# Performance work log

Measured on AMD Instinct MI355X. Metric: run time of the kernel, lower is better.

The kernel has to match this reference:

```python
import jax, jax.numpy as jnp
import numpy as np

N = 100000      # nodes
E = 1600000     # edges
F_IN = 512      # num_features
H = 128         # hidden
C = 40          # num_classes
K = 10          # Chebyshev order


def setup_inputs() -> dict:
    key = jax.random.key(0)
    ks = jax.random.split(key, 6)
    x = jax.random.normal(ks[0], (N, F_IN), dtype=jnp.float32)
    edge_index = jax.random.randint(ks[1], (2, E), 0, N, dtype=jnp.int32)
    W1 = jax.random.normal(ks[2], (F_IN, H), dtype=jnp.float32) / np.sqrt(F_IN).astype(np.float32)
    b1 = jnp.zeros((H,), dtype=jnp.float32)
    W2 = jax.random.normal(ks[3], (H, C), dtype=jnp.float32) / np.sqrt(H).astype(np.float32)
    b2 = jnp.zeros((C,), dtype=jnp.float32)
    # Chebyshev coefficients temp[K+1]
    temp = 1.0 + 0.1 * jax.random.normal(ks[4], (K + 1,), dtype=jnp.float32)
    return {"x": x, "edge_index": edge_index, "W1": W1, "b1": b1, "W2": W2, "b2": b2, "temp": temp}


def reference(x, edge_index, W1, b1, W2, b2, temp):
    # MLP encoder (eval mode: dropout is identity)
    h = jax.nn.relu(x @ W1 + b1)          # [N, H]
    h = h @ W2 + b2                        # [N, C]

    # gcn_norm: add self-loops, symmetric normalization
    self_loop = jnp.arange(N, dtype=edge_index.dtype)
    row = jnp.concatenate([edge_index[0], self_loop])   # [E+N]
    col = jnp.concatenate([edge_index[1], self_loop])
    deg = jax.ops.segment_sum(jnp.ones_like(row, dtype=jnp.float32), row, num_segments=N)
    dis = jnp.where(deg > 0, jax.lax.rsqrt(jnp.maximum(deg, 1.0)), 0.0)
    norm = dis[row] * dis[col]             # [E+N]

    def prop(v):  # A_hat @ v : gather-scale-scatter over edges
        return jax.ops.segment_sum(norm[:, None] * v[col], row, num_segments=N)

    # Chebyshev recurrence: Tx_k = 2*A_hat*Tx_{k-1} - Tx_{k-2}
    Tx0 = h
    Tx1 = prop(h)
    out0 = temp[0] * Tx0 + temp[1] * Tx1

    def body(carry, coe):
        t0, t1, acc = carry
        t2 = 2.0 * prop(t1) - t0
        return (t1, t2, acc + coe * t2), None

    (_, _, out), _ = jax.lax.scan(body, (Tx0, Tx1, out0), temp[2:])
    return jax.nn.log_softmax(out, axis=1)
```

## Files before the change

### kernel.cpp

```cpp
#include <hip/hip_runtime.h>
#include <hip/hip_bf16.h>
#include <cstdint>
#include <cstddef>

#define NN   100000
#define EE   1600000
#define FIN  512
#define HID  128
#define CC   40
#define KORD 10
#define SHB  80
#define SHSTRIDE ((size_t)NN * SHB)

typedef __attribute__((ext_vector_type(4))) float f4;
typedef __attribute__((ext_vector_type(8))) short short8_t;
typedef __attribute__((ext_vector_type(4))) unsigned int u4;

__device__ __forceinline__ unsigned short cvt_bf16(float f) {
  union { float f; unsigned u; } a; a.f = f;
  unsigned r = a.u + 0x7fffu + ((a.u >> 16) & 1u);
  return (unsigned short)(r >> 16);
}
__device__ __forceinline__ unsigned pk_bf(float a, float b) {
  union { float f; unsigned u; } x, y; x.f = a; y.f = b;
  unsigned ra = x.u + 0x7fffu + ((x.u >> 16) & 1u);
  unsigned rb = y.u + 0x7fffu + ((y.u >> 16) & 1u);
  return (ra >> 16) | (rb & 0xffff0000u);
}
__device__ __forceinline__ f4 cvf2(unsigned lo, unsigned hi) {
  union { unsigned u; float f; } a, b, c, d;
  a.u = lo << 16; b.u = lo & 0xffff0000u;
  c.u = hi << 16; d.u = hi & 0xffff0000u;
  f4 r; r.x = a.f; r.y = b.f; r.z = c.f; r.w = d.f; return r;
}

__global__ __launch_bounds__(256) void k_dw(const int* __restrict__ rowI, int* __restrict__ deg,
                                            const float* __restrict__ W1, unsigned short* __restrict__ W1T,
                                            int ndeg) {
  int b = blockIdx.x;
  if (b < ndeg) {
    int i = b * 256 + threadIdx.x;
    if (i < EE) atomicAdd(&deg[rowI[i]], 1);
  } else {
    int idx = (b - ndeg) * 256 + threadIdx.x;
    int k = idx >> 7, n = idx & 127;
    W1T[(k >> 5) * 4096 + n * 32 + (k & 31)] = cvt_bf16(W1[idx]);
  }
}

__global__ __launch_bounds__(256) void k_finalize(int* __restrict__ deg, float* __restrict__ dis,
                                                  float* __restrict__ sqd, float* __restrict__ invd) {
  int i = blockIdx.x * 256 + threadIdx.x;
  if (i < NN) {
    int d = deg[i] + 1;
    deg[i] = d;
    float fd = (float)d;
    dis[i]  = rsqrtf(fd);
    sqd[i]  = sqrtf(fd);
    invd[i] = 1.0f / fd;
  }
}

__global__ __launch_bounds__(256) void k_scan1(const int* __restrict__ cnt, int* __restrict__ excl,
                                               int* __restrict__ bsums) {
  __shared__ int s[256];
  int tid = threadIdx.x;
  int base = blockIdx.x * 1024 + tid * 4;
  int v0 = (base + 0 < NN) ? cnt[base + 0] : 0;
  int v1 = (base + 1 < NN) ? cnt[base + 1] : 0;
  int v2 = (base + 2 < NN) ? cnt[base + 2] : 0;
  int v3 = (base + 3 < NN) ? cnt[base + 3] : 0;
  int tsum = v0 + v1 + v2 + v3;
  s[tid] = tsum;
  __syncthreads();
  for (int off = 1; off < 256; off <<= 1) {
    int t = (tid >= off) ? s[tid - off] : 0;
    __syncthreads();
    if (tid >= off) s[tid] += t;
    __syncthreads();
  }
  int run = s[tid] - tsum;
  if (tid == 255) bsums[blockIdx.x] = s[255];
  if (base + 0 < NN) excl[base + 0] = run; run += v0;
  if (base + 1 < NN) excl[base + 1] = run; run += v1;
  if (base + 2 < NN) excl[base + 2] = run; run += v2;
  if (base + 3 < NN) excl[base + 3] = run;
}

__global__ __launch_bounds__(128) void k_scan2(int* __restrict__ bsums, int nb) {
  __shared__ int s[128];
  int tid = threadIdx.x;
  int v = (tid < nb) ? bsums[tid] : 0;
  s[tid] = v;
  __syncthreads();
  for (int off = 1; off < 128; off <<= 1) {
    int t = (tid >= off) ? s[tid - off] : 0;
    __syncthreads();
    if (tid >= off) s[tid] += t;
    __syncthreads();
  }
  if (tid < nb) bsums[tid] = s[tid] - v;
}

__global__ __launch_bounds__(256) void k_scan3(const int* __restrict__ cnt, int* __restrict__ rs,
                                               int* __restrict__ cur, const int* __restrict__ bsums) {
  int i = blockIdx.x * 256 + threadIdx.x;
  if (i < NN) {
    int v = rs[i] + bsums[i >> 10];
    rs[i] = v;
    cur[i] = v;
    if (i == NN - 1) rs[NN] = v + cnt[i];
  }
}

#define SLICE_ROWS (NN / 8)
#define SC_CHUNK   2048
__global__ __launch_bounds__(256) void k_scatter(const int* __restrict__ rowI, const int* __restrict__ colI,
                                                 int* __restrict__ cur, int* __restrict__ colS) {
  int slice = blockIdx.x & 7;
  int chunk = blockIdx.x >> 3;
  int lo = slice * SLICE_ROWS, hi = lo + SLICE_ROWS;
#pragma unroll
  for (int t = 0; t < SC_CHUNK / 256; ++t) {
    int i = chunk * SC_CHUNK + t * 256 + threadIdx.x;
    if (i < EE + NN) {
      int r = (i < EE) ? rowI[i] : (i - EE);
      if (r >= lo && r < hi) {
        int c = (i < EE) ? colI[i] : r;
        int pos = atomicAdd(&cur[r], 1);
        colS[pos] = c * SHB;
      }
    }
  }
}

#define LDK 40
__global__ __launch_bounds__(256) void k_gemm1(const float* __restrict__ x, const unsigned short* __restrict__ W1T,
                                               const float* __restrict__ b1, float* __restrict__ h1) {
  __shared__ __align__(16) short As_s[128][LDK];
  __shared__ __align__(16) short Bs_s[128][LDK];
  int tid  = threadIdx.x;
  int wave = tid >> 6, lane = tid & 63;
  int blockRow = blockIdx.x * 128;
  int wr = (wave & 1) * 64, wc = (wave >> 1) * 64;
  int l15 = lane & 15, lk = (lane >> 4) * 8;
  int ar = tid >> 1, ak = (tid & 1) * 16;

  f4 acc[4][4] = {};

  for (int k0 = 0; k0 < FIN; k0 += 32) {
    int gr = blockRow + ar;
    f4 xv0 = {0.f,0.f,0.f,0.f}, xv1 = xv0, xv2 = xv0, xv3 = xv0;
    if (gr < NN) {
      const float* xr = x + (size_t)gr * FIN + k0 + ak;
      xv0 = *(const f4*)&xr[0];
      xv1 = *(const f4*)&xr[4];
      xv2 = *(const f4*)&xr[8];
      xv3 = *(const f4*)&xr[12];
    }
    short8_t p0, p1;
#pragma unroll
    for (int q = 0; q < 4; ++q) {
      p0[q]     = (short)cvt_bf16(xv0[q]);
      p0[q + 4] = (short)cvt_bf16(xv1[q]);
      p1[q]     = (short)cvt_bf16(xv2[q]);
      p1[q + 4] = (short)cvt_bf16(xv3[q]);
    }
    *(short8_t*)&As_s[ar][ak]     = p0;
    *(short8_t*)&As_s[ar][ak + 8] = p1;

    const unsigned short* Wt = W1T + (k0 >> 5) * 4096;
    short8_t q0 = *(const short8_t*)&Wt[tid * 16];
    short8_t q1 = *(const short8_t*)&Wt[tid * 16 + 8];
    int bn = tid >> 1, bkk = (tid & 1) * 16;
    *(short8_t*)&Bs_s[bn][bkk]     = q0;
    *(short8_t*)&Bs_s[bn][bkk + 8] = q1;

    __syncthreads();

    short8_t afr[4], bfr[4];
#pragma unroll
    for (int m = 0; m < 4; ++m) afr[m] = *(const short8_t*)&As_s[wr + m * 16 + l15][lk];
#pragma unroll
    for (int n = 0; n < 4; ++n) bfr[n] = *(const short8_t*)&Bs_s[wc + n * 16 + l15][lk];
#pragma unroll
    for (int m = 0; m < 4; ++m)
#pragma unroll
      for (int n = 0; n < 4; ++n)
        acc[m][n] = __builtin_amdgcn_mfma_f32_16x16x32_bf16(afr[m], bfr[n], acc[m][n], 0, 0, 0);

    __syncthreads();
  }

  float bias[4];
#pragma unroll
  for (int n = 0; n < 4; ++n) bias[n] = b1[wc + n * 16 + l15];
#pragma unroll
  for (int m = 0; m < 4; ++m) {
    int baseRow = blockRow + wr + m * 16 + (lane >> 4) * 4;
#pragma unroll
    for (int n = 0; n < 4; ++n) {
      int col = wc + n * 16 + l15;
#pragma unroll
      for (int r = 0; r < 4; ++r) {
        int grow = baseRow + r;
        if (grow < NN) h1[(size_t)grow * HID + col] = fmaxf(acc[m][n][r] + bias[n], 0.f);
      }
    }
  }
}

__global__ __launch_bounds__(256) void k_gemm2(const float* __restrict__ h1, const float* __restrict__ W2,
                                               const float* __restrict__ b2, const float* __restrict__ temp,
                                               const float* __restrict__ dis,
                                               unsigned short* __restrict__ sh0) {
  __shared__ float sW[HID * CC];
  __shared__ float sb[CC];
  int tid = threadIdx.x;
  for (int i = tid; i < HID * CC; i += 256) sW[i] = W2[i];
  if (tid < CC) sb[tid] = b2[tid];
  __syncthreads();
  int gid = blockIdx.x * 256 + tid;
  if (gid >= NN * 20) return;
  int row = gid / 20;
  int c2  = (gid - row * 20) * 2;
  const float* hr = h1 + (size_t)row * HID;
  float a0 = sb[c2], a1 = sb[c2 + 1];
#pragma unroll 8
  for (int k = 0; k < HID; ++k) {
    float hv = hr[k];
    a0 = fmaf(hv, sW[k * CC + c2], a0);
    a1 = fmaf(hv, sW[k * CC + c2 + 1], a1);
  }
  float dv = dis[row];
  *(unsigned*)((char*)sh0 + (size_t)row * SHB + c2 * 2) = pk_bf(a0 * dv, a1 * dv);
}

template <int MODE>
__global__ __launch_bounds__(256) void k_prop(const unsigned short* __restrict__ shIn,
                                              const unsigned short* __restrict__ shPrev,
                                              unsigned short* __restrict__ shOut,
                                              const int* __restrict__ colS,
                                              const int* __restrict__ rs,
                                              const float* __restrict__ invd) {
  int lane = threadIdx.x & 63;
  int wave = threadIdx.x >> 6;
  int grp  = lane / 5;
  int fi   = lane - grp * 5;
  int node = blockIdx.x * 48 + wave * 12 + grp;
  bool active = (grp < 12) && (node < NN);
  int s = 0, e = 0;
  if (active) { s = rs[node]; e = rs[node + 1]; }
  const char* base = (const char*)shIn + fi * 16;
  f4 lo0 = {0.f,0.f,0.f,0.f}, hi0 = lo0, lo1 = lo0, hi1 = lo0;
  f4 lo2 = lo0, hi2 = lo0, lo3 = lo0, hi3 = lo0;
  int j = s;
  for (; j + 4 <= e; j += 4) {
    int c0 = colS[j], c1 = colS[j + 1], c2 = colS[j + 2], c3 = colS[j + 3];
    u4 p0 = *(const u4*)(base + c0);
    u4 p1 = *(const u4*)(base + c1);
    u4 p2 = *(const u4*)(base + c2);
    u4 p3 = *(const u4*)(base + c3);
    lo0 += cvf2(p0.x, p0.y); hi0 += cvf2(p0.z, p0.w);
    lo1 += cvf2(p1.x, p1.y); hi1 += cvf2(p1.z, p1.w);
    lo2 += cvf2(p2.x, p2.y); hi2 += cvf2(p2.z, p2.w);
    lo3 += cvf2(p3.x, p3.y); hi3 += cvf2(p3.z, p3.w);
  }
  if (j + 2 <= e) {
    int c0 = colS[j], c1 = colS[j + 1];
    u4 p0 = *(const u4*)(base + c0);
    u4 p1 = *(const u4*)(base + c1);
    lo0 += cvf2(p0.x, p0.y); hi0 += cvf2(p0.z, p0.w);
    lo1 += cvf2(p1.x, p1.y); hi1 += cvf2(p1.z, p1.w);
    j += 2;
  }
  if (j < e) {
    u4 p0 = *(const u4*)(base + colS[j]);
    lo2 += cvf2(p0.x, p0.y); hi2 += cvf2(p0.z, p0.w);
  }

  if (active) {
    f4 slo = (lo0 + lo1) + (lo2 + lo3);
    f4 shi = (hi0 + hi1) + (hi2 + hi3);
    float iv = invd[node];
    size_t ro = (size_t)node * SHB + fi * 16;
    f4 wlo, whi;
    if (MODE == 0) {
      wlo = iv * slo; whi = iv * shi;
    } else {
      u4 pp = *(const u4*)((const char*)shPrev + ro);
      f4 plo = cvf2(pp.x, pp.y), phi = cvf2(pp.z, pp.w);
      wlo = (2.f * iv) * slo - plo;
      whi = (2.f * iv) * shi - phi;
    }
    u4 pk;
    pk.x = pk_bf(wlo.x, wlo.y); pk.y = pk_bf(wlo.z, wlo.w);
    pk.z = pk_bf(whi.x, whi.y); pk.w = pk_bf(whi.z, whi.w);
    *(u4*)((char*)shOut + ro) = pk;
  }
}

__global__ __launch_bounds__(256) void k_comb(const unsigned short* __restrict__ shBase,
                                              float* __restrict__ outF,
                                              const float* __restrict__ sqd,
                                              const float* __restrict__ temp) {
  int lane = threadIdx.x & 63;
  int wave = threadIdx.x >> 6;
  int grp  = lane / 5;
  int fi   = lane - grp * 5;
  int node = blockIdx.x * 48 + wave * 12 + grp;
  if (grp >= 12 || node >= NN) return;

  const char* p = (const char*)shBase + (size_t)node * SHB + fi * 16;
  f4 alo = {0.f,0.f,0.f,0.f}, ahi = alo;
#pragma unroll
  for (int k = 0; k <= KORD; ++k) {
    u4 pp = *(const u4*)(p + (size_t)k * SHSTRIDE);
    float tk = temp[k];
    alo += tk * cvf2(pp.x, pp.y);
    ahi += tk * cvf2(pp.z, pp.w);
  }
  float sq = sqd[node];
  alo *= sq; ahi *= sq;

  int gb = grp * 5;
  float m = fmaxf(fmaxf(fmaxf(alo.x, alo.y), fmaxf(alo.z, alo.w)),
                  fmaxf(fmaxf(ahi.x, ahi.y), fmaxf(ahi.z, ahi.w)));
  float mm = m;
#pragma unroll
  for (int j = 0; j < 5; ++j) mm = fmaxf(mm, __shfl(m, gb + j));
  float ss = expf(alo.x - mm) + expf(alo.y - mm) + expf(alo.z - mm) + expf(alo.w - mm)
           + expf(ahi.x - mm) + expf(ahi.y - mm) + expf(ahi.z - mm) + expf(ahi.w - mm);
  float tot = 0.f;
#pragma unroll
  for (int j = 0; j < 5; ++j) tot += __shfl(ss, gb + j);
  float lse = mm + logf(tot);
  alo -= lse; ahi -= lse;
  size_t o = (size_t)node * CC + fi * 8;
  *(f4*)&outF[o]     = alo;
  *(f4*)&outF[o + 4] = ahi;
}

extern "C" void kernel_launch(void* const* d_in, const int* in_sizes, int n_in,
                              void* d_out, int out_size, void* d_ws, size_t ws_size,
                              hipStream_t stream) {
  const float* x    = (const float*)d_in[0];
  const int*   ei   = (const int*)d_in[1];
  const float* W1   = (const float*)d_in[2];
  const float* b1   = (const float*)d_in[3];
  const float* W2   = (const float*)d_in[4];
  const float* b2   = (const float*)d_in[5];
  const float* temp = (const float*)d_in[6];
  const int* rowI = ei;
  const int* colI = ei + EE;
  float* out = (float*)d_out;

  char* w = (char*)d_ws;
  auto alloc = [&](size_t bytes) -> void* {
    void* p = (void*)w;
    w += (bytes + 255) & ~(size_t)255;
    return p;
  };
  int*   deg   = (int*)  alloc((size_t)NN * 4);
  float* dis   = (float*)alloc((size_t)NN * 4);
  float* sqd   = (float*)alloc((size_t)NN * 4);
  float* invd  = (float*)alloc((size_t)NN * 4);
  int*   rs    = (int*)  alloc((size_t)(NN + 1) * 4);
  int*   cur   = (int*)  alloc((size_t)NN * 4);
  int*   bsums = (int*)  alloc(512 * 4);
  unsigned short* W1T = (unsigned short*)alloc((size_t)FIN * HID * 2);
  unsigned short* shAll = (unsigned short*)alloc(SHSTRIDE * (KORD + 1));
  int*   colS  = (int*)  alloc((size_t)(EE + NN) * 4);
  float* h1    = (float*)alloc((size_t)NN * HID * 4);

  auto sh = [&](int k) -> unsigned short* {
    return (unsigned short*)((char*)shAll + (size_t)k * SHSTRIDE);
  };

  hipMemsetAsync(deg, 0, (size_t)NN * 4, stream);

  const int NDEG = (EE + 255) / 256;
  const int NW1T = FIN * HID / 256;
  k_dw<<<NDEG + NW1T, 256, 0, stream>>>(rowI, deg, W1, W1T, NDEG);

  k_finalize<<<(NN + 255) / 256, 256, 0, stream>>>(deg, dis, sqd, invd);

  int nb = (NN + 1023) / 1024;
  k_scan1<<<nb, 256, 0, stream>>>(deg, rs, bsums);
  k_scan2<<<1, 128, 0, stream>>>(bsums, nb);
  k_scan3<<<(NN + 255) / 256, 256, 0, stream>>>(deg, rs, cur, bsums);

  const int NCH = (EE + NN + SC_CHUNK - 1) / SC_CHUNK;
  k_scatter<<<8 * NCH, 256, 0, stream>>>(rowI, colI, cur, colS);

  k_gemm1<<<(NN + 127) / 128, 256, 0, stream>>>(x, W1T, b1, h1);
  k_gemm2<<<(NN * 20 + 255) / 256, 256, 0, stream>>>(h1, W2, b2, temp, dis, sh(0));

  int G = (NN + 47) / 48;
  k_prop<0><<<G, 256, 0, stream>>>(sh(0), sh(0), sh(1), colS, rs, invd);
  for (int k = 2; k <= KORD; ++k) {
    k_prop<1><<<G, 256, 0, stream>>>(sh(k - 1), sh(k - 2), sh(k), colS, rs, invd);
  }

  k_comb<<<G, 256, 0, stream>>>(shAll, out, sqd, temp);
}
```

Before: 633.9 us.

## Fold degree finalize into scan, stage x via direct LDS loads, unroll prop by 8

Removes the separate k_finalize launch by computing deg+1 inside the scan kernels and writing dis/sqd/invd in k_scan3. In gemm1, x tiles are loaded straight into LDS as fp32 through global_load_lds with an XOR swizzle, and converted to bf16 by truncation (instead of round-to-nearest) when the fragments are read, which saves register staging and conversion work. The propagation gather loop is unrolled to 8 edges per step to keep more loads in flight. Truncation changes rounding slightly, and the fp32 LDS tile doubles the shared memory used for A.

```diff
diff --git a/kernel.cpp b/kernel.cpp
--- a/kernel.cpp
+++ b/kernel.cpp
@@ -26,6 +26,10 @@
   unsigned ra = x.u + 0x7fffu + ((x.u >> 16) & 1u);
   unsigned rb = y.u + 0x7fffu + ((y.u >> 16) & 1u);
   return (ra >> 16) | (rb & 0xffff0000u);
+}
+__device__ __forceinline__ unsigned pk_tr(float a, float b) {
+  union { float f; unsigned u; } x, y; x.f = a; y.f = b;
+  return (x.u >> 16) | (y.u & 0xffff0000u);
 }
 __device__ __forceinline__ f4 cvf2(unsigned lo, unsigned hi) {
   union { unsigned u; float f; } a, b, c, d;
@@ -48,28 +52,15 @@
   }
 }
 
-__global__ __launch_bounds__(256) void k_finalize(int* __restrict__ deg, float* __restrict__ dis,
-                                                  float* __restrict__ sqd, float* __restrict__ invd) {
-  int i = blockIdx.x * 256 + threadIdx.x;
-  if (i < NN) {
-    int d = deg[i] + 1;
-    deg[i] = d;
-    float fd = (float)d;
-    dis[i]  = rsqrtf(fd);
-    sqd[i]  = sqrtf(fd);
-    invd[i] = 1.0f / fd;
-  }
-}
-
 __global__ __launch_bounds__(256) void k_scan1(const int* __restrict__ cnt, int* __restrict__ excl,
                                                int* __restrict__ bsums) {
   __shared__ int s[256];
   int tid = threadIdx.x;
   int base = blockIdx.x * 1024 + tid * 4;
-  int v0 = (base + 0 < NN) ? cnt[base + 0] : 0;
-  int v1 = (base + 1 < NN) ? cnt[base + 1] : 0;
-  int v2 = (base + 2 < NN) ? cnt[base + 2] : 0;
-  int v3 = (base + 3 < NN) ? cnt[base + 3] : 0;
+  int v0 = (base + 0 < NN) ? cnt[base + 0] + 1 : 0;
+  int v1 = (base + 1 < NN) ? cnt[base + 1] + 1 : 0;
+  int v2 = (base + 2 < NN) ? cnt[base + 2] + 1 : 0;
+  int v3 = (base + 3 < NN) ? cnt[base + 3] + 1 : 0;
   int tsum = v0 + v1 + v2 + v3;
   s[tid] = tsum;
   __syncthreads();
@@ -103,13 +94,20 @@
 }
 
 __global__ __launch_bounds__(256) void k_scan3(const int* __restrict__ cnt, int* __restrict__ rs,
-                                               int* __restrict__ cur, const int* __restrict__ bsums) {
+                                               int* __restrict__ cur, const int* __restrict__ bsums,
+                                               float* __restrict__ dis, float* __restrict__ sqd,
+                                               float* __restrict__ invd) {
   int i = blockIdx.x * 256 + threadIdx.x;
   if (i < NN) {
     int v = rs[i] + bsums[i >> 10];
     rs[i] = v;
     cur[i] = v;
-    if (i == NN - 1) rs[NN] = v + cnt[i];
+    int d = cnt[i] + 1;
+    if (i == NN - 1) rs[NN] = v + d;
+    float fd = (float)d;
+    dis[i]  = rsqrtf(fd);
+    sqd[i]  = sqrtf(fd);
+    invd[i] = 1.0f / fd;
   }
 }
 
@@ -137,37 +135,33 @@
 #define LDK 40
 __global__ __launch_bounds__(256) void k_gemm1(const float* __restrict__ x, const unsigned short* __restrict__ W1T,
                                                const float* __restrict__ b1, float* __restrict__ h1) {
-  __shared__ __align__(16) short As_s[128][LDK];
+  __shared__ __align__(16) float As_f[128 * 32];
   __shared__ __align__(16) short Bs_s[128][LDK];
   int tid  = threadIdx.x;
   int wave = tid >> 6, lane = tid & 63;
   int blockRow = blockIdx.x * 128;
   int wr = (wave & 1) * 64, wc = (wave >> 1) * 64;
-  int l15 = lane & 15, lk = (lane >> 4) * 8;
-  int ar = tid >> 1, ak = (tid & 1) * 16;
+  int l15 = lane & 15, hi4 = lane >> 4;
+
+  int sr = (wave << 5) + (lane >> 3);
+  int sslot = lane & 7;
 
   f4 acc[4][4] = {};
 
   for (int k0 = 0; k0 < FIN; k0 += 32) {
-    int gr = blockRow + ar;
-    f4 xv0 = {0.f,0.f,0.f,0.f}, xv1 = xv0, xv2 = xv0, xv3 = xv0;
-    if (gr < NN) {
-      const float* xr = x + (size_t)gr * FIN + k0 + ak;
-      xv0 = *(const f4*)&xr[0];
-      xv1 = *(const f4*)&xr[4];
-      xv2 = *(const f4*)&xr[8];
-      xv3 = *(const f4*)&xr[12];
+#pragma unroll
+    for (int c = 0; c < 4; ++c) {
+      int row = sr + c * 8;
+      int gr = blockRow + row;
+      int lslot = sslot ^ (row & 7);
+      const float* gp = x + (size_t)gr * FIN + k0 + lslot * 4;
+      float* lp = &As_f[(wave << 10) + (c << 8)];
+      if (gr < NN) {
+        __builtin_amdgcn_global_load_lds(
+            (const __attribute__((address_space(1))) unsigned int*)gp,
+            (__attribute__((address_space(3))) unsigned int*)lp, 16, 0, 0);
+      }
     }
-    short8_t p0, p1;
-#pragma unroll
-    for (int q = 0; q < 4; ++q) {
-      p0[q]     = (short)cvt_bf16(xv0[q]);
-      p0[q + 4] = (short)cvt_bf16(xv1[q]);
-      p1[q]     = (short)cvt_bf16(xv2[q]);
-      p1[q + 4] = (short)cvt_bf16(xv3[q]);
-    }
-    *(short8_t*)&As_s[ar][ak]     = p0;
-    *(short8_t*)&As_s[ar][ak + 8] = p1;
 
     const unsigned short* Wt = W1T + (k0 >> 5) * 4096;
     short8_t q0 = *(const short8_t*)&Wt[tid * 16];
@@ -180,9 +174,19 @@
 
     short8_t afr[4], bfr[4];
 #pragma unroll
-    for (int m = 0; m < 4; ++m) afr[m] = *(const short8_t*)&As_s[wr + m * 16 + l15][lk];
-#pragma unroll
-    for (int n = 0; n < 4; ++n) bfr[n] = *(const short8_t*)&Bs_s[wc + n * 16 + l15][lk];
+    for (int m = 0; m < 4; ++m) {
+      int row = wr + m * 16 + l15;
+      int s0 = (hi4 * 2) ^ (row & 7);
+      int s1 = (hi4 * 2 + 1) ^ (row & 7);
+      f4 a0 = *(const f4*)&As_f[(row << 5) + s0 * 4];
+      f4 a1 = *(const f4*)&As_f[(row << 5) + s1 * 4];
+      u4 p;
+      p.x = pk_tr(a0.x, a0.y); p.y = pk_tr(a0.z, a0.w);
+      p.z = pk_tr(a1.x, a1.y); p.w = pk_tr(a1.z, a1.w);
+      afr[m] = *(short8_t*)&p;
+    }
+#pragma unroll
+    for (int n = 0; n < 4; ++n) bfr[n] = *(const short8_t*)&Bs_s[wc + n * 16 + l15][hi4 * 8];
 #pragma unroll
     for (int m = 0; m < 4; ++m)
 #pragma unroll
@@ -197,7 +201,7 @@
   for (int n = 0; n < 4; ++n) bias[n] = b1[wc + n * 16 + l15];
 #pragma unroll
   for (int m = 0; m < 4; ++m) {
-    int baseRow = blockRow + wr + m * 16 + (lane >> 4) * 4;
+    int baseRow = blockRow + wr + m * 16 + hi4 * 4;
 #pragma unroll
     for (int n = 0; n < 4; ++n) {
       int col = wc + n * 16 + l15;
@@ -255,7 +259,27 @@
   f4 lo0 = {0.f,0.f,0.f,0.f}, hi0 = lo0, lo1 = lo0, hi1 = lo0;
   f4 lo2 = lo0, hi2 = lo0, lo3 = lo0, hi3 = lo0;
   int j = s;
-  for (; j + 4 <= e; j += 4) {
+  for (; j + 8 <= e; j += 8) {
+    int c0 = colS[j],     c1 = colS[j + 1], c2 = colS[j + 2], c3 = colS[j + 3];
+    int c4 = colS[j + 4], c5 = colS[j + 5], c6 = colS[j + 6], c7 = colS[j + 7];
+    u4 p0 = *(const u4*)(base + c0);
+    u4 p1 = *(const u4*)(base + c1);
+    u4 p2 = *(const u4*)(base + c2);
+    u4 p3 = *(const u4*)(base + c3);
+    u4 p4 = *(const u4*)(base + c4);
+    u4 p5 = *(const u4*)(base + c5);
+    u4 p6 = *(const u4*)(base + c6);
+    u4 p7 = *(const u4*)(base + c7);
+    lo0 += cvf2(p0.x, p0.y); hi0 += cvf2(p0.z, p0.w);
+    lo1 += cvf2(p1.x, p1.y); hi1 += cvf2(p1.z, p1.w);
+    lo2 += cvf2(p2.x, p2.y); hi2 += cvf2(p2.z, p2.w);
+    lo3 += cvf2(p3.x, p3.y); hi3 += cvf2(p3.z, p3.w);
+    lo0 += cvf2(p4.x, p4.y); hi0 += cvf2(p4.z, p4.w);
+    lo1 += cvf2(p5.x, p5.y); hi1 += cvf2(p5.z, p5.w);
+    lo2 += cvf2(p6.x, p6.y); hi2 += cvf2(p6.z, p6.w);
+    lo3 += cvf2(p7.x, p7.y); hi3 += cvf2(p7.z, p7.w);
+  }
+  if (j + 4 <= e) {
     int c0 = colS[j], c1 = colS[j + 1], c2 = colS[j + 2], c3 = colS[j + 3];
     u4 p0 = *(const u4*)(base + c0);
     u4 p1 = *(const u4*)(base + c1);
@@ -265,11 +289,11 @@
     lo1 += cvf2(p1.x, p1.y); hi1 += cvf2(p1.z, p1.w);
     lo2 += cvf2(p2.x, p2.y); hi2 += cvf2(p2.z, p2.w);
     lo3 += cvf2(p3.x, p3.y); hi3 += cvf2(p3.z, p3.w);
+    j += 4;
   }
   if (j + 2 <= e) {
-    int c0 = colS[j], c1 = colS[j + 1];
-    u4 p0 = *(const u4*)(base + c0);
-    u4 p1 = *(const u4*)(base + c1);
+    u4 p0 = *(const u4*)(base + colS[j]);
+    u4 p1 = *(const u4*)(base + colS[j + 1]);
     lo0 += cvf2(p0.x, p0.y); hi0 += cvf2(p0.z, p0.w);
     lo1 += cvf2(p1.x, p1.y); hi1 += cvf2(p1.z, p1.w);
     j += 2;
@@ -383,12 +407,10 @@
   const int NW1T = FIN * HID / 256;
   k_dw<<<NDEG + NW1T, 256, 0, stream>>>(rowI, deg, W1, W1T, NDEG);
 
-  k_finalize<<<(NN + 255) / 256, 256, 0, stream>>>(deg, dis, sqd, invd);
-
   int nb = (NN + 1023) / 1024;
   k_scan1<<<nb, 256, 0, stream>>>(deg, rs, bsums);
   k_scan2<<<1, 128, 0, stream>>>(bsums, nb);
-  k_scan3<<<(NN + 255) / 256, 256, 0, stream>>>(deg, rs, cur, bsums);
+  k_scan3<<<(NN + 255) / 256, 256, 0, stream>>>(deg, rs, cur, bsums, dis, sqd, invd);
 
   const int NCH = (EE + NN + SC_CHUNK - 1) / SC_CHUNK;
   k_scatter<<<8 * NCH, 256, 0, stream>>>(rowI, colI, cur, colS);
```

Result: no change. 625.8 us (-1.3%).
